# Kernel optimization log

Hardware: AMD Instinct MI355X
Metric: run time of the kernel (lower is better)

## Reference

```python
import jax, jax.numpy as jnp
import numpy as np

MAX_VALUE = 127.0  # signed 8-bit: 2**(8-1)-1


def _quantize_int8(t, amax):
    # per-tensor symmetric quantization: round(x * 127/amax), clamped to [-127, 127]
    scale = MAX_VALUE / amax
    return jnp.clip(jnp.round(t * scale), -MAX_VALUE, MAX_VALUE).astype(jnp.int8)


def setup_inputs() -> dict:
    key = jax.random.key(0)
    k1, k2, k3 = jax.random.split(key, 3)
    N, K, M = 8192, 4096, 4096
    x = jax.random.normal(k1, (N, K), dtype=jnp.float32)
    weight = jax.random.normal(k2, (M, K), dtype=jnp.float32) * (1.0 / np.sqrt(K))
    bias = jax.random.normal(k3, (M,), dtype=jnp.float32) * (1.0 / np.sqrt(K))
    return {"x": x, "weight": weight, "bias": bias}


def reference(x, weight, bias):
    # amax from max-abs calibration (per-tensor), as TensorQuantizer would hold
    amax = jnp.max(jnp.abs(x))
    amax_w = jnp.max(jnp.abs(weight))
    qi = _quantize_int8(x, amax)          # [N, K] int8
    qw = _quantize_int8(weight, amax_w)   # [M, K] int8
    acc = jnp.matmul(qi.astype(jnp.int32), qw.astype(jnp.int32).T)  # [N, M] int32
    # dequant: output / ((max/amax) * (max/amax_w)), then bias
    dequant = (amax * amax_w) / (MAX_VALUE * MAX_VALUE)
    return acc.astype(jnp.float32) * dequant + bias
```

## Files before the change

### kernel.cpp

```cpp
#include <hip/hip_runtime.h>

#define K_DIM 4096
#define N_DIM 8192
#define M_DIM 4096

typedef int v4i __attribute__((ext_vector_type(4)));

__global__ void amax2_kernel(const float4* __restrict__ x,
                             const float4* __restrict__ w,
                             unsigned* __restrict__ scal) {
  const int XB = 2048, WB = 1024;
  const float4* p;
  int n4, b, nb;
  unsigned* out;
  if (blockIdx.x < XB) {
    p = x; n4 = N_DIM * K_DIM / 4; out = scal + 0; b = blockIdx.x; nb = XB;
  } else {
    p = w; n4 = M_DIM * K_DIM / 4; out = scal + 1; b = blockIdx.x - XB; nb = WB;
  }
  int tid = b * blockDim.x + threadIdx.x;
  int stride = nb * blockDim.x;
  float m = 0.f;
  for (int i = tid; i < n4; i += stride) {
    float4 v = p[i];
    m = fmaxf(m, fmaxf(fmaxf(fabsf(v.x), fabsf(v.y)),
                       fmaxf(fabsf(v.z), fabsf(v.w))));
  }
#pragma unroll
  for (int off = 32; off > 0; off >>= 1)
    m = fmaxf(m, __shfl_down(m, off));
  __shared__ float sm[4];
  int lane = threadIdx.x & 63, wv = threadIdx.x >> 6;
  if (lane == 0) sm[wv] = m;
  __syncthreads();
  if (threadIdx.x == 0) {
    m = fmaxf(fmaxf(sm[0], sm[1]), fmaxf(sm[2], sm[3]));
    atomicMax(out, __float_as_uint(m));
  }
}

__device__ __forceinline__ unsigned pack4(float4 v, float s) {
  int q0 = (int)fminf(fmaxf(rintf(v.x * s), -127.f), 127.f);
  int q1 = (int)fminf(fmaxf(rintf(v.y * s), -127.f), 127.f);
  int q2 = (int)fminf(fmaxf(rintf(v.z * s), -127.f), 127.f);
  int q3 = (int)fminf(fmaxf(rintf(v.w * s), -127.f), 127.f);
  return (unsigned)(q0 & 255) | ((unsigned)(q1 & 255) << 8) |
         ((unsigned)(q2 & 255) << 16) | ((unsigned)(q3 & 255) << 24);
}

__global__ void quant2_kernel(const float4* __restrict__ x,
                              const float4* __restrict__ w,
                              unsigned* __restrict__ qx, unsigned* __restrict__ qw,
                              const unsigned* __restrict__ scal) {
  const int XB = 2048, WB = 1024;
  const float4* in;
  unsigned* out;
  int n4, b, nb;
  float amax;
  if (blockIdx.x < XB) {
    in = x; out = qx; n4 = N_DIM * K_DIM / 4; b = blockIdx.x; nb = XB;
    amax = __uint_as_float(scal[0]);
  } else {
    in = w; out = qw; n4 = M_DIM * K_DIM / 4; b = blockIdx.x - XB; nb = WB;
    amax = __uint_as_float(scal[1]);
  }
  float s = 127.0f / amax;
  int tid = b * blockDim.x + threadIdx.x;
  int stride = nb * blockDim.x;
  for (int i = tid; i < n4; i += stride) out[i] = pack4(in[i], s);
}

__device__ __forceinline__ void gld_lds16(const void* g, void* l) {
  __builtin_amdgcn_global_load_lds(
      (const __attribute__((address_space(1))) void*)g,
      (__attribute__((address_space(3))) void*)l, 16, 0, 0);
}

__global__ __launch_bounds__(512, 2) void gemm_i8(
    const signed char* __restrict__ A,
    const signed char* __restrict__ B,
    const float* __restrict__ bias,
    float* __restrict__ out,
    const unsigned* __restrict__ scal)
{
  __shared__ signed char lds[4][2][128 * 128];

  const int tid = threadIdx.x;
  const int lane = tid & 63;
  const int w = tid >> 6;
  const int wm = w >> 2;
  const int wn = w & 3;

  const int bid = blockIdx.x;
  const int xcd = bid & 7, idx = bid >> 3;
  const int bx = (xcd & 3) * 8 + (idx & 7);
  const int by = (xcd >> 2) * 8 + (idx >> 3);
  const long r0 = (long)bx * 256;
  const long c0 = (long)by * 256;

  const int u = (tid & 7) ^ ((tid >> 3) & 7);
  const long sR = (long)(u >> 2) * 128 + (tid >> 3);
  const int scol = (u & 3) * 16;
  const signed char* gA = A + (r0 + sR) * K_DIM + scol;
  const signed char* gB = B + (c0 + sR) * K_DIM + scol;
  const int ldst = tid * 16;

  v4i acc[8][4];
#pragma unroll
  for (int i = 0; i < 8; ++i)
#pragma unroll
    for (int j = 0; j < 4; ++j) acc[i][j] = (v4i){0, 0, 0, 0};

  const int fr = lane & 15;
  const int fq = lane >> 4;
  const int sw = fr & 7;

  const int aoff = fr * 128 + (((wm << 2) | fq) ^ sw) * 16;
  const int boff = ((wn & 1) * 64 + fr) * 128 + ((((wn >> 1) << 2) | fq) ^ sw) * 16;

  auto STAGE = [&](int T, int p) {
    signed char* la = &lds[T & 3][0][0];
    signed char* lb = &lds[T & 3][1][0];
    gld_lds16(gA + (long)p * 64 * K_DIM + T * 64, la + p * 8192 + ldst);
    gld_lds16(gB + (long)p * 64 * K_DIM + T * 64, lb + p * 8192 + ldst);
  };

  auto TILE = [&](int T, bool stg, int guard) {
    const signed char* la = &lds[T & 3][0][0];
    const signed char* lb = &lds[T & 3][1][0];
    v4i bv[4], a0[4], a1[4];
#pragma unroll
    for (int nf = 0; nf < 4; ++nf)
      bv[nf] = *(const v4i*)(lb + boff + nf * 2048);
#pragma unroll
    for (int mi = 0; mi < 4; ++mi)
      a0[mi] = *(const v4i*)(la + aoff + mi * 2048);
    if (stg) STAGE(T + 3, 0);
    __builtin_amdgcn_s_barrier();
    asm volatile("s_waitcnt lgkmcnt(0)" ::: "memory");
    __builtin_amdgcn_s_setprio(1);
#pragma unroll
    for (int mi = 0; mi < 4; ++mi)
#pragma unroll
      for (int nf = 0; nf < 4; ++nf)
        acc[mi][nf] = __builtin_amdgcn_mfma_i32_16x16x64_i8(a0[mi], bv[nf],
                                                            acc[mi][nf], 0, 0, 0);
    __builtin_amdgcn_s_setprio(0);
    __builtin_amdgcn_s_barrier();
#pragma unroll
    for (int mi = 0; mi < 4; ++mi)
      a1[mi] = *(const v4i*)(la + aoff + 8192 + mi * 2048);
    if (stg) STAGE(T + 3, 1);
    if (guard == 8) asm volatile("s_waitcnt vmcnt(8)" ::: "memory");
    else if (guard == 4) asm volatile("s_waitcnt vmcnt(4)" ::: "memory");
    else if (guard == 0) asm volatile("s_waitcnt vmcnt(0)" ::: "memory");
    __builtin_amdgcn_s_barrier();
    asm volatile("s_waitcnt lgkmcnt(0)" ::: "memory");
    __builtin_amdgcn_s_setprio(1);
#pragma unroll
    for (int mi = 0; mi < 4; ++mi)
#pragma unroll
      for (int nf = 0; nf < 4; ++nf)
        acc[4 + mi][nf] = __builtin_amdgcn_mfma_i32_16x16x64_i8(
            a1[mi], bv[nf], acc[4 + mi][nf], 0, 0, 0);
    __builtin_amdgcn_s_setprio(0);
    __builtin_amdgcn_s_barrier();
  };

  const int NT = K_DIM / 64;
#pragma unroll
  for (int T = 0; T < 3; ++T) { STAGE(T, 0); STAGE(T, 1); }
  asm volatile("s_waitcnt vmcnt(8)" ::: "memory");
  __builtin_amdgcn_s_barrier();

#pragma unroll 1
  for (int T = 0; T + 4 <= NT; ++T) TILE(T, true, 8);
  TILE(NT - 3, false, 4);
  TILE(NT - 2, false, 0);
  TILE(NT - 1, false, -1);

  const float dq =
      (__uint_as_float(scal[0]) * __uint_as_float(scal[1])) / 16129.0f;
  float bs[4];
#pragma unroll
  for (int nf = 0; nf < 4; ++nf) bs[nf] = bias[c0 + wn * 64 + nf * 16 + fr];

#pragma unroll
  for (int mf = 0; mf < 8; ++mf) {
    const long rbase = r0 + wm * 128 + mf * 16 + fq * 4;
#pragma unroll
    for (int nf = 0; nf < 4; ++nf) {
      const long c = c0 + wn * 64 + nf * 16 + fr;
#pragma unroll
      for (int t = 0; t < 4; ++t) {
        out[(rbase + t) * (long)M_DIM + c] = (float)acc[mf][nf][t] * dq + bs[nf];
      }
    }
  }
}

extern "C" void kernel_launch(void* const* d_in, const int* in_sizes, int n_in,
                              void* d_out, int out_size, void* d_ws, size_t ws_size,
                              hipStream_t stream) {
  const float* x = (const float*)d_in[0];
  const float* wt = (const float*)d_in[1];
  const float* bias = (const float*)d_in[2];
  float* out = (float*)d_out;

  unsigned* scal = (unsigned*)d_ws;
  signed char* qx = (signed char*)d_ws + 256;
  signed char* qw = qx + (long)N_DIM * K_DIM;

  hipMemsetAsync(d_ws, 0, 16, stream);

  amax2_kernel<<<3072, 256, 0, stream>>>((const float4*)x, (const float4*)wt,
                                         scal);
  quant2_kernel<<<3072, 256, 0, stream>>>((const float4*)x, (const float4*)wt,
                                          (unsigned*)qx, (unsigned*)qw, scal);

  gemm_i8<<<512, 512, 0, stream>>>(qx, qw, bias, out, scal);
}
```

Measured before the change: 434.6 us.

## Use one barrier per K-tile in the int8 GEMM and unroll amax/quant loops

The GEMM main loop now waits on vmcnt and hits one barrier at the start of each K-tile. It then reads all eight A fragments, issues both halves of the next stage's global-to-LDS loads together, and runs all 32 MFMAs in a single burst. This replaces the earlier two-half schedule, which used four barriers per tile. The amax and quantize kernels swap their grid-stride loops for fully unrolled, fixed-trip-count loops with two independent max accumulators, to get more loads in flight. The trade-off is that the GEMM holds more fragment registers at once and has less overlap between LDS reads and MFMA work inside a tile.

```diff
diff --git a/kernel.cpp b/kernel.cpp
--- a/kernel.cpp
+++ b/kernel.cpp
@@ -9,23 +9,34 @@
 __global__ void amax2_kernel(const float4* __restrict__ x,
                              const float4* __restrict__ w,
                              unsigned* __restrict__ scal) {
-  const int XB = 2048, WB = 1024;
-  const float4* p;
-  int n4, b, nb;
+  float m0 = 0.f, m1 = 0.f;
   unsigned* out;
-  if (blockIdx.x < XB) {
-    p = x; n4 = N_DIM * K_DIM / 4; out = scal + 0; b = blockIdx.x; nb = XB;
+  if (blockIdx.x < 2048) {
+    const long base = (long)blockIdx.x * 256 + threadIdx.x;
+#pragma unroll
+    for (int k = 0; k < 16; k += 2) {
+      float4 a = x[base + (long)k * 524288];
+      float4 b = x[base + (long)(k + 1) * 524288];
+      m0 = fmaxf(m0, fmaxf(fmaxf(fabsf(a.x), fabsf(a.y)),
+                           fmaxf(fabsf(a.z), fabsf(a.w))));
+      m1 = fmaxf(m1, fmaxf(fmaxf(fabsf(b.x), fabsf(b.y)),
+                           fmaxf(fabsf(b.z), fabsf(b.w))));
+    }
+    out = scal + 0;
   } else {
-    p = w; n4 = M_DIM * K_DIM / 4; out = scal + 1; b = blockIdx.x - XB; nb = WB;
-  }
-  int tid = b * blockDim.x + threadIdx.x;
-  int stride = nb * blockDim.x;
-  float m = 0.f;
-  for (int i = tid; i < n4; i += stride) {
-    float4 v = p[i];
-    m = fmaxf(m, fmaxf(fmaxf(fabsf(v.x), fabsf(v.y)),
-                       fmaxf(fabsf(v.z), fabsf(v.w))));
-  }
+    const long base = (long)(blockIdx.x - 2048) * 256 + threadIdx.x;
+#pragma unroll
+    for (int k = 0; k < 16; k += 2) {
+      float4 a = w[base + (long)k * 262144];
+      float4 b = w[base + (long)(k + 1) * 262144];
+      m0 = fmaxf(m0, fmaxf(fmaxf(fabsf(a.x), fabsf(a.y)),
+                           fmaxf(fabsf(a.z), fabsf(a.w))));
+      m1 = fmaxf(m1, fmaxf(fmaxf(fabsf(b.x), fabsf(b.y)),
+                           fmaxf(fabsf(b.z), fabsf(b.w))));
+    }
+    out = scal + 1;
+  }
+  float m = fmaxf(m0, m1);
 #pragma unroll
   for (int off = 32; off > 0; off >>= 1)
     m = fmaxf(m, __shfl_down(m, off));
@@ -52,22 +63,19 @@
                               const float4* __restrict__ w,
                               unsigned* __restrict__ qx, unsigned* __restrict__ qw,
                               const unsigned* __restrict__ scal) {
-  const int XB = 2048, WB = 1024;
-  const float4* in;
-  unsigned* out;
-  int n4, b, nb;
-  float amax;
-  if (blockIdx.x < XB) {
-    in = x; out = qx; n4 = N_DIM * K_DIM / 4; b = blockIdx.x; nb = XB;
-    amax = __uint_as_float(scal[0]);
+  if (blockIdx.x < 2048) {
+    const float s = 127.0f / __uint_as_float(scal[0]);
+    const long base = (long)blockIdx.x * 256 + threadIdx.x;
+#pragma unroll
+    for (int k = 0; k < 16; ++k)
+      qx[base + (long)k * 524288] = pack4(x[base + (long)k * 524288], s);
   } else {
-    in = w; out = qw; n4 = M_DIM * K_DIM / 4; b = blockIdx.x - XB; nb = WB;
-    amax = __uint_as_float(scal[1]);
-  }
-  float s = 127.0f / amax;
-  int tid = b * blockDim.x + threadIdx.x;
-  int stride = nb * blockDim.x;
-  for (int i = tid; i < n4; i += stride) out[i] = pack4(in[i], s);
+    const float s = 127.0f / __uint_as_float(scal[1]);
+    const long base = (long)(blockIdx.x - 2048) * 256 + threadIdx.x;
+#pragma unroll
+    for (int k = 0; k < 16; ++k)
+      qw[base + (long)k * 262144] = pack4(w[base + (long)k * 262144], s);
+  }
 }
 
 __device__ __forceinline__ void gld_lds16(const void* g, void* l) {
@@ -126,58 +134,42 @@
   };
 
   auto TILE = [&](int T, bool stg, int guard) {
+    if (guard == 8) asm volatile("s_waitcnt vmcnt(8)" ::: "memory");
+    else if (guard == 4) asm volatile("s_waitcnt vmcnt(4)" ::: "memory");
+    else asm volatile("s_waitcnt vmcnt(0)" ::: "memory");
+    __builtin_amdgcn_s_barrier();
     const signed char* la = &lds[T & 3][0][0];
     const signed char* lb = &lds[T & 3][1][0];
-    v4i bv[4], a0[4], a1[4];
+    v4i bv[4], av[8];
 #pragma unroll
     for (int nf = 0; nf < 4; ++nf)
       bv[nf] = *(const v4i*)(lb + boff + nf * 2048);
 #pragma unroll
     for (int mi = 0; mi < 4; ++mi)
-      a0[mi] = *(const v4i*)(la + aoff + mi * 2048);
-    if (stg) STAGE(T + 3, 0);
-    __builtin_amdgcn_s_barrier();
-    asm volatile("s_waitcnt lgkmcnt(0)" ::: "memory");
+      av[mi] = *(const v4i*)(la + aoff + mi * 2048);
+#pragma unroll
+    for (int mi = 0; mi < 4; ++mi)
+      av[4 + mi] = *(const v4i*)(la + aoff + 8192 + mi * 2048);
+    if (stg) { STAGE(T + 3, 0); STAGE(T + 3, 1); }
     __builtin_amdgcn_s_setprio(1);
 #pragma unroll
-    for (int mi = 0; mi < 4; ++mi)
+    for (int mi = 0; mi < 8; ++mi)
 #pragma unroll
       for (int nf = 0; nf < 4; ++nf)
-        acc[mi][nf] = __builtin_amdgcn_mfma_i32_16x16x64_i8(a0[mi], bv[nf],
+        acc[mi][nf] = __builtin_amdgcn_mfma_i32_16x16x64_i8(av[mi], bv[nf],
                                                             acc[mi][nf], 0, 0, 0);
     __builtin_amdgcn_s_setprio(0);
-    __builtin_amdgcn_s_barrier();
-#pragma unroll
-    for (int mi = 0; mi < 4; ++mi)
-      a1[mi] = *(const v4i*)(la + aoff + 8192 + mi * 2048);
-    if (stg) STAGE(T + 3, 1);
-    if (guard == 8) asm volatile("s_waitcnt vmcnt(8)" ::: "memory");
-    else if (guard == 4) asm volatile("s_waitcnt vmcnt(4)" ::: "memory");
-    else if (guard == 0) asm volatile("s_waitcnt vmcnt(0)" ::: "memory");
-    __builtin_amdgcn_s_barrier();
-    asm volatile("s_waitcnt lgkmcnt(0)" ::: "memory");
-    __builtin_amdgcn_s_setprio(1);
-#pragma unroll
-    for (int mi = 0; mi < 4; ++mi)
-#pragma unroll
-      for (int nf = 0; nf < 4; ++nf)
-        acc[4 + mi][nf] = __builtin_amdgcn_mfma_i32_16x16x64_i8(
-            a1[mi], bv[nf], acc[4 + mi][nf], 0, 0, 0);
-    __builtin_amdgcn_s_setprio(0);
-    __builtin_amdgcn_s_barrier();
   };
 
   const int NT = K_DIM / 64;
 #pragma unroll
   for (int T = 0; T < 3; ++T) { STAGE(T, 0); STAGE(T, 1); }
-  asm volatile("s_waitcnt vmcnt(8)" ::: "memory");
-  __builtin_amdgcn_s_barrier();
 
 #pragma unroll 1
-  for (int T = 0; T + 4 <= NT; ++T) TILE(T, true, 8);
-  TILE(NT - 3, false, 4);
-  TILE(NT - 2, false, 0);
-  TILE(NT - 1, false, -1);
+  for (int T = 0; T < NT - 3; ++T) TILE(T, true, 8);
+  TILE(NT - 3, false, 8);
+  TILE(NT - 2, false, 4);
+  TILE(NT - 1, false, 0);
 
   const float dq =
       (__uint_as_float(scal[0]) * __uint_as_float(scal[1])) / 16129.0f;
```

Result: no change. 435.1 us (+0.1%).

## Shrink GEMM tile to 256x128 with 3-stage LDS ring and higher occupancy

Applied to the files above, without the earlier changes.

The int8 GEMM block tile shrinks from 256x256 to 256x128, with 8 waves arranged 4x2, each owning a 64x64 sub-tile. The LDS ring drops from 4 buffers to 3 (72KB total), the grid doubles to 1024 blocks, and launch bounds request 4 blocks per CU. The pipeline becomes one wait-and-barrier per K tile instead of two half-tile phases, meant to raise occupancy and cut synchronisation. In exchange, arithmetic intensity per block falls, and the 4-blocks target (4 x 72KB of LDS) may not fit in LDS, so realised occupancy may be lower than requested.

```diff
diff --git a/kernel.cpp b/kernel.cpp
--- a/kernel.cpp
+++ b/kernel.cpp
@@ -76,38 +76,39 @@
       (__attribute__((address_space(3))) void*)l, 16, 0, 0);
 }
 
-__global__ __launch_bounds__(512, 2) void gemm_i8(
+__global__ __launch_bounds__(512, 4) void gemm_i8(
     const signed char* __restrict__ A,
     const signed char* __restrict__ B,
     const float* __restrict__ bias,
     float* __restrict__ out,
     const unsigned* __restrict__ scal)
 {
-  __shared__ signed char lds[4][2][128 * 128];
+  __shared__ signed char lds[3][24 * 1024];
 
   const int tid = threadIdx.x;
   const int lane = tid & 63;
   const int w = tid >> 6;
-  const int wm = w >> 2;
-  const int wn = w & 3;
+  const int wm4 = w >> 1;
+  const int wn2 = w & 1;
 
   const int bid = blockIdx.x;
   const int xcd = bid & 7, idx = bid >> 3;
   const int bx = (xcd & 3) * 8 + (idx & 7);
-  const int by = (xcd >> 2) * 8 + (idx >> 3);
+  const int by = (xcd >> 2) * 16 + (idx >> 3);
   const long r0 = (long)bx * 256;
-  const long c0 = (long)by * 256;
+  const long c0 = (long)by * 128;
 
   const int u = (tid & 7) ^ ((tid >> 3) & 7);
-  const long sR = (long)(u >> 2) * 128 + (tid >> 3);
+  const long sRa = (long)(u >> 2) * 128 + (tid >> 3);
+  const long sRb = (long)(u >> 2) * 64 + (tid >> 3);
   const int scol = (u & 3) * 16;
-  const signed char* gA = A + (r0 + sR) * K_DIM + scol;
-  const signed char* gB = B + (c0 + sR) * K_DIM + scol;
+  const signed char* gA = A + (r0 + sRa) * K_DIM + scol;
+  const signed char* gB = B + (c0 + sRb) * K_DIM + scol;
   const int ldst = tid * 16;
 
-  v4i acc[8][4];
-#pragma unroll
-  for (int i = 0; i < 8; ++i)
+  v4i acc[4][4];
+#pragma unroll
+  for (int i = 0; i < 4; ++i)
 #pragma unroll
     for (int j = 0; j < 4; ++j) acc[i][j] = (v4i){0, 0, 0, 0};
 
@@ -115,85 +116,64 @@
   const int fq = lane >> 4;
   const int sw = fr & 7;
 
-  const int aoff = fr * 128 + (((wm << 2) | fq) ^ sw) * 16;
-  const int boff = ((wn & 1) * 64 + fr) * 128 + ((((wn >> 1) << 2) | fq) ^ sw) * 16;
-
-  auto STAGE = [&](int T, int p) {
-    signed char* la = &lds[T & 3][0][0];
-    signed char* lb = &lds[T & 3][1][0];
-    gld_lds16(gA + (long)p * 64 * K_DIM + T * 64, la + p * 8192 + ldst);
-    gld_lds16(gB + (long)p * 64 * K_DIM + T * 64, lb + p * 8192 + ldst);
+  const int aoff = ((wm4 & 1) * 64 + fr) * 128 +
+                   ((((wm4 >> 1) << 2) | fq) ^ sw) * 16;
+  const int boff = 16384 + fr * 128 + (((wn2 << 2) | fq) ^ sw) * 16;
+
+  auto STAGE = [&](int T) {
+    signed char* base = &lds[T % 3][0];
+    const long ko = (long)T * 64;
+    gld_lds16(gA + ko, base + ldst);
+    gld_lds16(gA + 64 * K_DIM + ko, base + 8192 + ldst);
+    gld_lds16(gB + ko, base + 16384 + ldst);
   };
 
   auto TILE = [&](int T, bool stg, int guard) {
-    const signed char* la = &lds[T & 3][0][0];
-    const signed char* lb = &lds[T & 3][1][0];
-    v4i bv[4], a0[4], a1[4];
+    if (guard == 3) asm volatile("s_waitcnt vmcnt(3)" ::: "memory");
+    else asm volatile("s_waitcnt vmcnt(0)" ::: "memory");
+    __builtin_amdgcn_s_barrier();
+    const signed char* base = &lds[T % 3][0];
+    v4i av[4], bv[4];
 #pragma unroll
     for (int nf = 0; nf < 4; ++nf)
-      bv[nf] = *(const v4i*)(lb + boff + nf * 2048);
+      bv[nf] = *(const v4i*)(base + boff + nf * 2048);
 #pragma unroll
     for (int mi = 0; mi < 4; ++mi)
-      a0[mi] = *(const v4i*)(la + aoff + mi * 2048);
-    if (stg) STAGE(T + 3, 0);
-    __builtin_amdgcn_s_barrier();
-    asm volatile("s_waitcnt lgkmcnt(0)" ::: "memory");
+      av[mi] = *(const v4i*)(base + aoff + mi * 2048);
+    if (stg) STAGE(T + 2);
     __builtin_amdgcn_s_setprio(1);
 #pragma unroll
     for (int mi = 0; mi < 4; ++mi)
 #pragma unroll
       for (int nf = 0; nf < 4; ++nf)
-        acc[mi][nf] = __builtin_amdgcn_mfma_i32_16x16x64_i8(a0[mi], bv[nf],
+        acc[mi][nf] = __builtin_amdgcn_mfma_i32_16x16x64_i8(av[mi], bv[nf],
                                                             acc[mi][nf], 0, 0, 0);
     __builtin_amdgcn_s_setprio(0);
-    __builtin_amdgcn_s_barrier();
-#pragma unroll
-    for (int mi = 0; mi < 4; ++mi)
-      a1[mi] = *(const v4i*)(la + aoff + 8192 + mi * 2048);
-    if (stg) STAGE(T + 3, 1);
-    if (guard == 8) asm volatile("s_waitcnt vmcnt(8)" ::: "memory");
-    else if (guard == 4) asm volatile("s_waitcnt vmcnt(4)" ::: "memory");
-    else if (guard == 0) asm volatile("s_waitcnt vmcnt(0)" ::: "memory");
-    __builtin_amdgcn_s_barrier();
-    asm volatile("s_waitcnt lgkmcnt(0)" ::: "memory");
-    __builtin_amdgcn_s_setprio(1);
-#pragma unroll
-    for (int mi = 0; mi < 4; ++mi)
-#pragma unroll
-      for (int nf = 0; nf < 4; ++nf)
-        acc[4 + mi][nf] = __builtin_amdgcn_mfma_i32_16x16x64_i8(
-            a1[mi], bv[nf], acc[4 + mi][nf], 0, 0, 0);
-    __builtin_amdgcn_s_setprio(0);
-    __builtin_amdgcn_s_barrier();
   };
 
   const int NT = K_DIM / 64;
-#pragma unroll
-  for (int T = 0; T < 3; ++T) { STAGE(T, 0); STAGE(T, 1); }
-  asm volatile("s_waitcnt vmcnt(8)" ::: "memory");
-  __builtin_amdgcn_s_barrier();
-
+  STAGE(0);
+  STAGE(1);
 #pragma unroll 1
-  for (int T = 0; T + 4 <= NT; ++T) TILE(T, true, 8);
-  TILE(NT - 3, false, 4);
-  TILE(NT - 2, false, 0);
-  TILE(NT - 1, false, -1);
+  for (int T = 0; T < NT - 2; ++T) TILE(T, true, 3);
+  TILE(NT - 2, false, 3);
+  TILE(NT - 1, false, 0);
 
   const float dq =
       (__uint_as_float(scal[0]) * __uint_as_float(scal[1])) / 16129.0f;
   float bs[4];
 #pragma unroll
-  for (int nf = 0; nf < 4; ++nf) bs[nf] = bias[c0 + wn * 64 + nf * 16 + fr];
-
-#pragma unroll
-  for (int mf = 0; mf < 8; ++mf) {
-    const long rbase = r0 + wm * 128 + mf * 16 + fq * 4;
+  for (int nf = 0; nf < 4; ++nf) bs[nf] = bias[c0 + wn2 * 64 + nf * 16 + fr];
+
+#pragma unroll
+  for (int mi = 0; mi < 4; ++mi) {
+    const long rbase = r0 + wm4 * 64 + mi * 16 + fq * 4;
 #pragma unroll
     for (int nf = 0; nf < 4; ++nf) {
-      const long c = c0 + wn * 64 + nf * 16 + fr;
+      const long c = c0 + wn2 * 64 + nf * 16 + fr;
 #pragma unroll
       for (int t = 0; t < 4; ++t) {
-        out[(rbase + t) * (long)M_DIM + c] = (float)acc[mf][nf][t] * dq + bs[nf];
+        out[(rbase + t) * (long)M_DIM + c] = (float)acc[mi][nf][t] * dq + bs[nf];
       }
     }
   }
@@ -218,5 +198,5 @@
   quant2_kernel<<<3072, 256, 0, stream>>>((const float4*)x, (const float4*)wt,
                                           (unsigned*)qx, (unsigned*)qw, scal);
 
-  gemm_i8<<<512, 512, 0, stream>>>(qx, qw, bias, out, scal);
-}
+  gemm_i8<<<1024, 512, 0, stream>>>(qx, qw, bias, out, scal);
+}
```

Result: slower. 449.2 us (+3.4%).
